# Performance work log

Measured on AMD Instinct MI355X. Metric: run time of the kernel, lower is better.

Reference implementation:

```python
import jax, jax.numpy as jnp
import numpy as np

D_MODEL = 1024
HEADS = 16
D_K = D_MODEL // HEADS  # 64
LN_EPS = 1e-5


def setup_inputs() -> dict:
    key = jax.random.key(0)
    ks = jax.random.split(key, 9)
    B, S = 4, 2048
    x = jax.random.normal(ks[0], (B, S, D_MODEL), dtype=jnp.float32)
    s = 1.0 / np.sqrt(D_K)
    # Per-head linear weights, stacked over heads: [H, d_in, d_out]
    Wq = jax.random.uniform(ks[1], (HEADS, D_K, D_K), jnp.float32, -s, s)
    Wk = jax.random.uniform(ks[2], (HEADS, D_K, D_K), jnp.float32, -s, s)
    Wv = jax.random.uniform(ks[3], (HEADS, D_K, D_K), jnp.float32, -s, s)
    bq = jax.random.uniform(ks[4], (HEADS, D_K), jnp.float32, -s, s)
    bk = jax.random.uniform(ks[5], (HEADS, D_K), jnp.float32, -s, s)
    bv = jax.random.uniform(ks[6], (HEADS, D_K), jnp.float32, -s, s)
    gamma = jnp.ones((D_MODEL,), jnp.float32)
    beta = jnp.zeros((D_MODEL,), jnp.float32)
    return {"x": x, "Wq": Wq, "Wk": Wk, "Wv": Wv,
            "bq": bq, "bk": bk, "bv": bv, "gamma": gamma, "beta": beta}


def reference(x, Wq, Wk, Wv, bq, bk, bv, gamma, beta):
    B, S, D = x.shape
    scale = jnp.sqrt(jnp.asarray(D_K, x.dtype))
    # chunk(x, heads, -1) == reshape to [B,S,H,d_k]
    xh = x.reshape(B, S, HEADS, D_K)
    # Batched per-head linears (replaces the Python loop over heads)
    Q = jnp.einsum('bshd,hde->bshe', xh, Wq) + bq  # [B,S,H,d_k]
    K = jnp.einsum('bshd,hde->bshe', xh, Wk) + bk
    V = jnp.einsum('bshd,hde->bshe', xh, Wv) + bv
    scores = jnp.einsum('bshd,bthd->bhst', Q, K) / scale  # [B,H,S,S]
    A = jax.nn.softmax(scores, axis=-1)
    out = jnp.einsum('bhst,bthd->bshd', A, V).reshape(B, S, D)
    # dropout is identity in eval mode; residual + LayerNorm
    y = out + x
    mu = jnp.mean(y, axis=-1, keepdims=True)
    var = jnp.mean((y - mu) ** 2, axis=-1, keepdims=True)
    return (y - mu) * jax.lax.rsqrt(var + LN_EPS) * gamma + beta
```

## Files before the change

### kernel.cpp

```cpp
#include <hip/hip_runtime.h>
#include <math.h>

typedef __bf16 bf16_t;
typedef __bf16 bf16x8 __attribute__((ext_vector_type(8)));
typedef __bf16 bf16x4 __attribute__((ext_vector_type(4)));
typedef short short4v __attribute__((ext_vector_type(4)));
typedef float f32x4 __attribute__((ext_vector_type(4)));

#define LOG2E 1.4426950408889634f

#if __has_builtin(__builtin_amdgcn_exp2f)
#define FAST_EXP2(x) __builtin_amdgcn_exp2f(x)
#else
#define FAST_EXP2(x) exp2f(x)
#endif

#define GLOBAL_AS __attribute__((address_space(1)))
#define LDS_AS    __attribute__((address_space(3)))

__device__ __forceinline__ void async_ld16(const void* g, void* l) {
    __builtin_amdgcn_global_load_lds((const GLOBAL_AS void*)g,
                                     (LDS_AS void*)l, 16, 0, 0);
}

constexpr int BATCH = 4;
constexpr int SEQ = 2048;
constexpr int NHEADS = 16;
constexpr int DK = 64;
constexpr int DMODEL = 1024;
constexpr int NTOK = BATCH * SEQ;

constexpr size_t WT_OFF   = 0;
constexpr size_t BIAS_OFF = WT_OFF + (size_t)3*16*64*64*2;
constexpr size_t Q_OFF    = BIAS_OFF + (size_t)3*16*64*4;
constexpr size_t QSZ      = (size_t)BATCH*NHEADS*SEQ*DK*2;
constexpr size_t K_OFF    = Q_OFF + QSZ;
constexpr size_t VT_OFF   = K_OFF + QSZ;
constexpr size_t O_OFF    = VT_OFF + QSZ;

__global__ __launch_bounds__(256) void prep_kernel(
    const float* __restrict__ Wq, const float* __restrict__ Wk,
    const float* __restrict__ Wv, const float* __restrict__ bq,
    const float* __restrict__ bk, const float* __restrict__ bv,
    bf16_t* __restrict__ Wt, float* __restrict__ bias)
{
    const float QS = 0.125f * LOG2E;
    int i = blockIdx.x * 256 + threadIdx.x;
    if (i < 3*16*64*64) {
        int d = i & 63, e = (i >> 6) & 63, h = (i >> 12) & 15, p = i >> 16;
        const float* W = (p == 0) ? Wq : (p == 1) ? Wk : Wv;
        float v = W[(h*64 + d)*64 + e] * ((p == 0) ? QS : 1.0f);
        Wt[i] = (bf16_t)v;
    }
    if (i < 3*16*64) {
        int e = i & 63, h = (i >> 6) & 15, p = i >> 10;
        const float* bb = (p == 0) ? bq : (p == 1) ? bk : bv;
        bias[i] = bb[h*64 + e] * ((p == 0) ? QS : 1.0f);
    }
}

__global__ __launch_bounds__(256) void qkv_kernel(
    const float* __restrict__ x, const bf16_t* __restrict__ Wt,
    const float* __restrict__ bias,
    bf16_t* __restrict__ Q, bf16_t* __restrict__ Kg, bf16_t* __restrict__ Vt)
{
    constexpr int QSTR = 72;
    __shared__ bf16_t Slds[4][16 * QSTR];
    const int tid = threadIdx.x;
    const int w = tid >> 6, lane = tid & 63;
    const int ln = lane & 15, quad = lane >> 4;
    const int gw = blockIdx.x * 4 + w;
    const int h = gw & 15, tt = gw >> 4;
    const int t0 = tt * 16;
    const int b = t0 >> 11;
    const int s0 = t0 & 2047;
    const int bh = b * 16 + h;

    bf16x8 afrag[2];
#pragma unroll
    for (int kc = 0; kc < 2; kc++) {
        const float* xp = &x[(size_t)(t0 + ln)*DMODEL + h*DK + kc*32 + quad*8];
        float4 u0 = *(const float4*)xp;
        float4 u1 = *(const float4*)(xp + 4);
        bf16x8 a;
        a[0]=(bf16_t)u0.x; a[1]=(bf16_t)u0.y; a[2]=(bf16_t)u0.z; a[3]=(bf16_t)u0.w;
        a[4]=(bf16_t)u1.x; a[5]=(bf16_t)u1.y; a[6]=(bf16_t)u1.z; a[7]=(bf16_t)u1.w;
        afrag[kc] = a;
    }

#pragma unroll
    for (int p = 0; p < 3; p++) {
#pragma unroll
        for (int nt = 0; nt < 4; nt++) {
            const bf16_t* wp = &Wt[((size_t)((p*16 + h)*64) + nt*16 + ln)*64 + quad*8];
            bf16x8 b0 = *(const bf16x8*)wp;
            bf16x8 b1 = *(const bf16x8*)(wp + 32);
            f32x4 acc = {0.f, 0.f, 0.f, 0.f};
            acc = __builtin_amdgcn_mfma_f32_16x16x32_bf16(afrag[0], b0, acc, 0, 0, 0);
            acc = __builtin_amdgcn_mfma_f32_16x16x32_bf16(afrag[1], b1, acc, 0, 0, 0);
            float bv = bias[(p*16 + h)*64 + nt*16 + ln];
#pragma unroll
            for (int r = 0; r < 4; r++)
                Slds[w][(quad*4 + r)*QSTR + nt*16 + ln] = (bf16_t)(acc[r] + bv);
        }
        if (p < 2) {
            bf16_t* dst = (p == 0) ? Q : Kg;
            const int row = lane >> 2, c = (lane & 3) * 16;
            bf16_t* dp = &dst[((size_t)bh*SEQ + s0 + row)*DK + c];
            *(uint4*)dp       = *(const uint4*)&Slds[w][row*QSTR + c];
            *(uint4*)(dp + 8) = *(const uint4*)&Slds[w][row*QSTR + c + 8];
        } else {
            unsigned int packed[8];
#pragma unroll
            for (int i = 0; i < 8; i++) {
                unsigned short lo = __builtin_bit_cast(unsigned short, Slds[w][(2*i  )*QSTR + lane]);
                unsigned short hi = __builtin_bit_cast(unsigned short, Slds[w][(2*i+1)*QSTR + lane]);
                packed[i] = (unsigned)lo | ((unsigned)hi << 16);
            }
            bf16_t* vp = &Vt[((size_t)bh*DK + lane)*SEQ + s0];
            uint4 v0; v0.x = packed[0]; v0.y = packed[1]; v0.z = packed[2]; v0.w = packed[3];
            uint4 v1; v1.x = packed[4]; v1.y = packed[5]; v1.z = packed[6]; v1.w = packed[7];
            *(uint4*)(vp)     = v0;
            *(uint4*)(vp + 8) = v1;
        }
    }
}

__global__ __launch_bounds__(256, 4) void flash_kernel(
    const bf16_t* __restrict__ Q, const bf16_t* __restrict__ Kg,
    const bf16_t* __restrict__ Vt, bf16_t* __restrict__ O)
{
    __shared__ union {
        struct { bf16_t K[2][64*64]; bf16_t V[2][64*64]; } kv;
        bf16_t O[4][32 * 72];
    } sh;

    const int tid = threadIdx.x;
    const int w = tid >> 6, lane = tid & 63;
    const int ln = lane & 15, quad = lane >> 4;
    const int bid = blockIdx.x;
    const int xcd = bid & 7;
    const int j   = bid >> 3;
    const int bh  = xcd * 8 + (j & 7);
    const int qt  = j >> 3;
    const int q0 = qt * 128 + w * 32;

    const bf16_t* kbase = &Kg[(size_t)bh * SEQ * DK];
    const bf16_t* vbase = &Vt[(size_t)bh * DK * SEQ];

    const int lrow = lane >> 3;
    const int swz  = ((lane & 7) ^ lrow) * 8;

    auto stage = [&](int ci, int buf) {
#pragma unroll
        for (int jj = 0; jj < 2; jj++) {
            const int r = w*16 + jj*8 + lrow;
            async_ld16(&kbase[(size_t)(ci*64 + r)*DK + swz],
                       &sh.kv.K[buf][(w*16 + jj*8)*64]);
            async_ld16(&vbase[(size_t)r*SEQ + ci*64 + swz],
                       &sh.kv.V[buf][(w*16 + jj*8)*64]);
        }
    };

    bf16x8 qfrag[2][2];
#pragma unroll
    for (int st = 0; st < 2; st++)
#pragma unroll
        for (int kc = 0; kc < 2; kc++)
            qfrag[st][kc] = *(const bf16x8*)
                &Q[((size_t)bh*SEQ + q0 + st*16 + ln)*DK + kc*32 + quad*8];

    f32x4 o[2][4];
#pragma unroll
    for (int st = 0; st < 2; st++)
#pragma unroll
        for (int dt = 0; dt < 4; dt++)
            o[st][dt] = (f32x4){0.f, 0.f, 0.f, 0.f};
    float l_[2] = {0.f, 0.f};

    const int s7  = ln & 7;
    const int kc0 = (quad ^ s7) * 8;
    const int vq  = quad >> 1;
    const int vo  = (quad & 1) * 4;

    constexpr int NC = SEQ / 64;
    stage(0, 0);

#pragma unroll 2
    for (int ci = 0; ci < NC; ci++) {
        asm volatile("s_waitcnt vmcnt(0)" ::: "memory");
        __syncthreads();
        if (ci + 1 < NC) stage(ci + 1, (ci + 1) & 1);

        const bf16_t* Kb = sh.kv.K[ci & 1];
        const bf16_t* Vb = sh.kv.V[ci & 1];

        f32x4 sfrag[2][4];
#pragma unroll
        for (int kt = 0; kt < 4; kt++) {
            const int kr = (kt*16 + ln) * 64;
            bf16x8 ka0 = *(const bf16x8*)&Kb[kr + kc0];
            bf16x8 ka1 = *(const bf16x8*)&Kb[kr + (kc0 ^ 32)];
#pragma unroll
            for (int st = 0; st < 2; st++) {
                f32x4 acc = {0.f, 0.f, 0.f, 0.f};
                acc = __builtin_amdgcn_mfma_f32_16x16x32_bf16(ka0, qfrag[st][0], acc, 0, 0, 0);
                acc = __builtin_amdgcn_mfma_f32_16x16x32_bf16(ka1, qfrag[st][1], acc, 0, 0, 0);
                sfrag[st][kt] = acc;
            }
        }

        bf16x8 pfrag[2][2];
#pragma unroll
        for (int st = 0; st < 2; st++) {
            float sum = 0.f;
            unsigned pk[8];
#pragma unroll
            for (int kt = 0; kt < 4; kt++) {
                float e0 = FAST_EXP2(sfrag[st][kt][0]);
                float e1 = FAST_EXP2(sfrag[st][kt][1]);
                float e2 = FAST_EXP2(sfrag[st][kt][2]);
                float e3 = FAST_EXP2(sfrag[st][kt][3]);
                sum += (e0 + e1) + (e2 + e3);
                unsigned u0 = __builtin_bit_cast(unsigned, e0);
                unsigned u1 = __builtin_bit_cast(unsigned, e1);
                unsigned u2 = __builtin_bit_cast(unsigned, e2);
                unsigned u3 = __builtin_bit_cast(unsigned, e3);
                pk[2*kt]     = __builtin_amdgcn_perm(u1, u0, 0x07060302);
                pk[2*kt + 1] = __builtin_amdgcn_perm(u3, u2, 0x07060302);
            }
            l_[st] += sum;
            uint4 lo; lo.x = pk[0]; lo.y = pk[1]; lo.z = pk[2]; lo.w = pk[3];
            uint4 hi; hi.x = pk[4]; hi.y = pk[5]; hi.z = pk[6]; hi.w = pk[7];
            pfrag[st][0] = __builtin_bit_cast(bf16x8, lo);
            pfrag[st][1] = __builtin_bit_cast(bf16x8, hi);
        }

#pragma unroll
        for (int kt2 = 0; kt2 < 2; kt2++) {
#pragma unroll
            for (int dt = 0; dt < 4; dt++) {
                const int vr = (dt*16 + ln) * 64;
                uint2 va0 = *(const uint2*)
                    &Vb[vr + (((kt2*4 + vq) ^ s7) * 8) + vo];
                uint2 va1 = *(const uint2*)
                    &Vb[vr + (((kt2*4 + 2 + vq) ^ s7) * 8) + vo];
                uint4 vv; vv.x = va0.x; vv.y = va0.y; vv.z = va1.x; vv.w = va1.y;
                bf16x8 va = __builtin_bit_cast(bf16x8, vv);
                o[0][dt] = __builtin_amdgcn_mfma_f32_16x16x32_bf16(
                    va, pfrag[0][kt2], o[0][dt], 0, 0, 0);
                o[1][dt] = __builtin_amdgcn_mfma_f32_16x16x32_bf16(
                    va, pfrag[1][kt2], o[1][dt], 0, 0, 0);
            }
        }
    }

    __syncthreads();
#pragma unroll
    for (int st = 0; st < 2; st++) {
        float l = l_[st];
        l += __shfl_xor(l, 16);
        l += __shfl_xor(l, 32);
        float rl = 1.0f / l;
#pragma unroll
        for (int dt = 0; dt < 4; dt++)
#pragma unroll
            for (int r = 0; r < 4; r++)
                sh.O[w][(st*16 + ln)*72 + dt*16 + quad*4 + r] =
                    (bf16_t)(o[st][dt][r] * rl);
    }
    const int token = lane >> 1, half = lane & 1;
    const int b = bh >> 4, h = bh & 15;
    const size_t s = (size_t)q0 + token;
    bf16_t* op = &O[(((size_t)b*SEQ + s)*NHEADS + h)*DK + half*32];
#pragma unroll
    for (int k2 = 0; k2 < 4; k2++)
        *(uint4*)(op + k2*8) = *(const uint4*)&sh.O[w][token*72 + half*32 + k2*8];
}

__global__ __launch_bounds__(256) void ln_kernel(
    const bf16_t* __restrict__ O, const float* __restrict__ x,
    const float* __restrict__ gamma, const float* __restrict__ beta,
    float* __restrict__ out)
{
    const int tid = threadIdx.x;
    const int w = tid >> 6, lane = tid & 63;
    const size_t t = (size_t)blockIdx.x * 4 + w;
    const int d0 = lane * 16;
    const bf16_t* op = &O[t*DMODEL + d0];
    const float* xp = &x[t*DMODEL + d0];

    bf16x8 oa = *(const bf16x8*)op;
    bf16x8 ob = *(const bf16x8*)(op + 8);
    float xs[16];
    ((float4*)xs)[0] = *(const float4*)(xp);
    ((float4*)xs)[1] = *(const float4*)(xp + 4);
    ((float4*)xs)[2] = *(const float4*)(xp + 8);
    ((float4*)xs)[3] = *(const float4*)(xp + 12);

    float yv[16];
    float sum = 0.f, sq = 0.f;
#pragma unroll
    for (int j = 0; j < 16; j++) {
        float ov = (j < 8) ? (float)oa[j] : (float)ob[j - 8];
        yv[j] = ov + xs[j];
        sum += yv[j];
        sq += yv[j] * yv[j];
    }
#pragma unroll
    for (int off = 1; off < 64; off <<= 1) {
        sum += __shfl_xor(sum, off);
        sq  += __shfl_xor(sq, off);
    }
    float mean = sum * (1.0f / DMODEL);
    float var = sq * (1.0f / DMODEL) - mean * mean;
    float rstd = rsqrtf(var + 1e-5f);

    float gs[16], bs[16];
    ((float4*)gs)[0] = *(const float4*)&gamma[d0];
    ((float4*)gs)[1] = *(const float4*)&gamma[d0 + 4];
    ((float4*)gs)[2] = *(const float4*)&gamma[d0 + 8];
    ((float4*)gs)[3] = *(const float4*)&gamma[d0 + 12];
    ((float4*)bs)[0] = *(const float4*)&beta[d0];
    ((float4*)bs)[1] = *(const float4*)&beta[d0 + 4];
    ((float4*)bs)[2] = *(const float4*)&beta[d0 + 8];
    ((float4*)bs)[3] = *(const float4*)&beta[d0 + 12];

    float res[16];
#pragma unroll
    for (int j = 0; j < 16; j++)
        res[j] = (yv[j] - mean) * rstd * gs[j] + bs[j];
    float* outp = &out[t*DMODEL + d0];
    *(float4*)(outp)      = *(float4*)&res[0];
    *(float4*)(outp + 4)  = *(float4*)&res[4];
    *(float4*)(outp + 8)  = *(float4*)&res[8];
    *(float4*)(outp + 12) = *(float4*)&res[12];
}

extern "C" void kernel_launch(void* const* d_in, const int* in_sizes, int n_in,
                              void* d_out, int out_size, void* d_ws, size_t ws_size,
                              hipStream_t stream) {
    const float* x     = (const float*)d_in[0];
    const float* Wq    = (const float*)d_in[1];
    const float* Wk    = (const float*)d_in[2];
    const float* Wv    = (const float*)d_in[3];
    const float* bq    = (const float*)d_in[4];
    const float* bk    = (const float*)d_in[5];
    const float* bv    = (const float*)d_in[6];
    const float* gamma = (const float*)d_in[7];
    const float* beta  = (const float*)d_in[8];

    char* ws = (char*)d_ws;
    bf16_t* Wt   = (bf16_t*)(ws + WT_OFF);
    float*  bias = (float*)(ws + BIAS_OFF);
    bf16_t* Qb   = (bf16_t*)(ws + Q_OFF);
    bf16_t* Kb   = (bf16_t*)(ws + K_OFF);
    bf16_t* Vtb  = (bf16_t*)(ws + VT_OFF);
    bf16_t* Ob   = (bf16_t*)(ws + O_OFF);

    prep_kernel<<<768, 256, 0, stream>>>(Wq, Wk, Wv, bq, bk, bv, Wt, bias);
    qkv_kernel<<<NTOK*NHEADS/16/4, 256, 0, stream>>>(x, Wt, bias, Qb, Kb, Vtb);
    flash_kernel<<<BATCH*NHEADS*(SEQ/128), 256, 0, stream>>>(Qb, Kb, Vtb, Ob);
    ln_kernel<<<NTOK/4, 256, 0, stream>>>(Ob, x, gamma, beta, (float*)d_out);
}
```

Measured before the change: 221.7 us.

## Software-pipeline QK^T ahead of softmax/PV with triple-buffered V and repacked V layout

Restructures the flash attention main loop so that QK^T for the next key chunk is computed while the softmax and PV for the current chunk proceed. A third V buffer and a two-chunk prefetch distance keep loads ahead of compute, and s_setprio is raised around the PV MFMAs. The V-transpose writer also stores V in an interleaved 32-column layout, so the PV A-fragment becomes one 16-byte LDS read instead of two 8-byte reads. The cost is more LDS and higher register pressure from keeping two score tiles live, which could hurt occupancy under the 256x4 launch bounds.

```diff
diff --git a/kernel.cpp b/kernel.cpp
--- a/kernel.cpp
+++ b/kernel.cpp
@@ -117,11 +117,14 @@
                 unsigned short hi = __builtin_bit_cast(unsigned short, Slds[w][(2*i+1)*QSTR + lane]);
                 packed[i] = (unsigned)lo | ((unsigned)hi << 16);
             }
-            bf16_t* vp = &Vt[((size_t)bh*DK + lane)*SEQ + s0];
-            uint4 v0; v0.x = packed[0]; v0.y = packed[1]; v0.z = packed[2]; v0.w = packed[3];
-            uint4 v1; v1.x = packed[4]; v1.y = packed[5]; v1.z = packed[6]; v1.w = packed[7];
-            *(uint4*)(vp)     = v0;
-            *(uint4*)(vp + 8) = v1;
+            const int base32 = s0 & ~31;
+            const int pr = (s0 >> 4) & 1;
+            unsigned* vp32 = (unsigned*)&Vt[((size_t)bh*DK + lane)*SEQ + base32];
+#pragma unroll
+            for (int i2 = 0; i2 < 4; i2++) {
+                uint2 u; u.x = packed[2*i2]; u.y = packed[2*i2 + 1];
+                *(uint2*)(vp32 + i2*4 + pr*2) = u;
+            }
         }
     }
 }
@@ -131,7 +134,7 @@
     const bf16_t* __restrict__ Vt, bf16_t* __restrict__ O)
 {
     __shared__ union {
-        struct { bf16_t K[2][64*64]; bf16_t V[2][64*64]; } kv;
+        struct { bf16_t K[2][64*64]; bf16_t V[3][64*64]; } kv;
         bf16_t O[4][32 * 72];
     } sh;
 
@@ -151,14 +154,18 @@
     const int lrow = lane >> 3;
     const int swz  = ((lane & 7) ^ lrow) * 8;
 
-    auto stage = [&](int ci, int buf) {
+    auto stageK = [&](int ci, bf16_t* dst) {
 #pragma unroll
         for (int jj = 0; jj < 2; jj++) {
             const int r = w*16 + jj*8 + lrow;
-            async_ld16(&kbase[(size_t)(ci*64 + r)*DK + swz],
-                       &sh.kv.K[buf][(w*16 + jj*8)*64]);
-            async_ld16(&vbase[(size_t)r*SEQ + ci*64 + swz],
-                       &sh.kv.V[buf][(w*16 + jj*8)*64]);
+            async_ld16(&kbase[(size_t)(ci*64 + r)*DK + swz], dst + (w*16 + jj*8)*64);
+        }
+    };
+    auto stageV = [&](int ci, bf16_t* dst) {
+#pragma unroll
+        for (int jj = 0; jj < 2; jj++) {
+            const int r = w*16 + jj*8 + lrow;
+            async_ld16(&vbase[(size_t)r*SEQ + ci*64 + swz], dst + (w*16 + jj*8)*64);
         }
     };
 
@@ -180,22 +187,10 @@
 
     const int s7  = ln & 7;
     const int kc0 = (quad ^ s7) * 8;
-    const int vq  = quad >> 1;
-    const int vo  = (quad & 1) * 4;
 
     constexpr int NC = SEQ / 64;
-    stage(0, 0);
-
-#pragma unroll 2
-    for (int ci = 0; ci < NC; ci++) {
-        asm volatile("s_waitcnt vmcnt(0)" ::: "memory");
-        __syncthreads();
-        if (ci + 1 < NC) stage(ci + 1, (ci + 1) & 1);
-
-        const bf16_t* Kb = sh.kv.K[ci & 1];
-        const bf16_t* Vb = sh.kv.V[ci & 1];
-
-        f32x4 sfrag[2][4];
+
+    auto qkt = [&](const bf16_t* Kb, f32x4 (&sf)[2][4]) {
 #pragma unroll
         for (int kt = 0; kt < 4; kt++) {
             const int kr = (kt*16 + ln) * 64;
@@ -206,21 +201,22 @@
                 f32x4 acc = {0.f, 0.f, 0.f, 0.f};
                 acc = __builtin_amdgcn_mfma_f32_16x16x32_bf16(ka0, qfrag[st][0], acc, 0, 0, 0);
                 acc = __builtin_amdgcn_mfma_f32_16x16x32_bf16(ka1, qfrag[st][1], acc, 0, 0, 0);
-                sfrag[st][kt] = acc;
-            }
-        }
-
-        bf16x8 pfrag[2][2];
+                sf[st][kt] = acc;
+            }
+        }
+    };
+
+    auto sm = [&](f32x4 (&sf)[2][4], bf16x8 (&pf)[2][2]) {
 #pragma unroll
         for (int st = 0; st < 2; st++) {
             float sum = 0.f;
             unsigned pk[8];
 #pragma unroll
             for (int kt = 0; kt < 4; kt++) {
-                float e0 = FAST_EXP2(sfrag[st][kt][0]);
-                float e1 = FAST_EXP2(sfrag[st][kt][1]);
-                float e2 = FAST_EXP2(sfrag[st][kt][2]);
-                float e3 = FAST_EXP2(sfrag[st][kt][3]);
+                float e0 = FAST_EXP2(sf[st][kt][0]);
+                float e1 = FAST_EXP2(sf[st][kt][1]);
+                float e2 = FAST_EXP2(sf[st][kt][2]);
+                float e3 = FAST_EXP2(sf[st][kt][3]);
                 sum += (e0 + e1) + (e2 + e3);
                 unsigned u0 = __builtin_bit_cast(unsigned, e0);
                 unsigned u1 = __builtin_bit_cast(unsigned, e1);
@@ -232,26 +228,62 @@
             l_[st] += sum;
             uint4 lo; lo.x = pk[0]; lo.y = pk[1]; lo.z = pk[2]; lo.w = pk[3];
             uint4 hi; hi.x = pk[4]; hi.y = pk[5]; hi.z = pk[6]; hi.w = pk[7];
-            pfrag[st][0] = __builtin_bit_cast(bf16x8, lo);
-            pfrag[st][1] = __builtin_bit_cast(bf16x8, hi);
-        }
-
+            pf[st][0] = __builtin_bit_cast(bf16x8, lo);
+            pf[st][1] = __builtin_bit_cast(bf16x8, hi);
+        }
+    };
+
+    auto pv = [&](const bf16_t* Vb, bf16x8 (&pf)[2][2]) {
 #pragma unroll
         for (int kt2 = 0; kt2 < 2; kt2++) {
 #pragma unroll
             for (int dt = 0; dt < 4; dt++) {
                 const int vr = (dt*16 + ln) * 64;
-                uint2 va0 = *(const uint2*)
-                    &Vb[vr + (((kt2*4 + vq) ^ s7) * 8) + vo];
-                uint2 va1 = *(const uint2*)
-                    &Vb[vr + (((kt2*4 + 2 + vq) ^ s7) * 8) + vo];
-                uint4 vv; vv.x = va0.x; vv.y = va0.y; vv.z = va1.x; vv.w = va1.y;
-                bf16x8 va = __builtin_bit_cast(bf16x8, vv);
+                bf16x8 va = *(const bf16x8*)&Vb[vr + (((kt2*4 + quad) ^ s7) * 8)];
                 o[0][dt] = __builtin_amdgcn_mfma_f32_16x16x32_bf16(
-                    va, pfrag[0][kt2], o[0][dt], 0, 0, 0);
+                    va, pf[0][kt2], o[0][dt], 0, 0, 0);
                 o[1][dt] = __builtin_amdgcn_mfma_f32_16x16x32_bf16(
-                    va, pfrag[1][kt2], o[1][dt], 0, 0, 0);
-            }
+                    va, pf[1][kt2], o[1][dt], 0, 0, 0);
+            }
+        }
+    };
+
+    stageK(0, sh.kv.K[0]); stageV(0, sh.kv.V[0]);
+    stageK(1, sh.kv.K[1]); stageV(1, sh.kv.V[1]);
+    __syncthreads();
+
+    f32x4 sA[2][4], sB[2][4];
+    qkt(sh.kv.K[0], sA);
+
+    bf16_t* vcur = sh.kv.V[0];
+    bf16_t* vnxt = sh.kv.V[1];
+    bf16_t* vfar = sh.kv.V[2];
+
+    for (int cc = 0; cc < NC; cc += 2) {
+        {
+            asm volatile("s_waitcnt vmcnt(0)" ::: "memory");
+            __syncthreads();
+            if (cc + 2 < NC) { stageK(cc + 2, sh.kv.K[0]); stageV(cc + 2, vfar); }
+            bf16x8 pf[2][2];
+            sm(sA, pf);
+            qkt(sh.kv.K[1], sB);
+            __builtin_amdgcn_s_setprio(1);
+            pv(vcur, pf);
+            __builtin_amdgcn_s_setprio(0);
+            bf16_t* t = vcur; vcur = vnxt; vnxt = vfar; vfar = t;
+        }
+        {
+            const int c = cc + 1;
+            asm volatile("s_waitcnt vmcnt(0)" ::: "memory");
+            __syncthreads();
+            if (c + 2 < NC) { stageK(c + 2, sh.kv.K[1]); stageV(c + 2, vfar); }
+            bf16x8 pf[2][2];
+            sm(sB, pf);
+            if (c + 1 < NC) qkt(sh.kv.K[0], sA);
+            __builtin_amdgcn_s_setprio(1);
+            pv(vcur, pf);
+            __builtin_amdgcn_s_setprio(0);
+            bf16_t* t = vcur; vcur = vnxt; vnxt = vfar; vfar = t;
         }
     }
 
```

New measurement: 625.7 us. +182.2%, slower.

## Permute V layout to match MFMA fragments, stage x tile in LDS, raise MFMA priority

Applied to the files above, without the earlier changes.

The QKV kernel now has each block cover four heads of a 16-token tile. It loads the x tile cooperatively into LDS as bf16, so global reads are coalesced and contiguous. V^T is written in an interleaved per-32-token layout so the flash kernel can load each V fragment as one 16-byte LDS read instead of two 8-byte reads. The PV MFMA loop is wrapped in s_setprio to favour matrix issue. This adds a block barrier and a second LDS buffer in the QKV kernel, and it relies on the producer and consumer agreeing on the permuted V layout.

```diff
diff --git a/kernel.cpp b/kernel.cpp
--- a/kernel.cpp
+++ b/kernel.cpp
@@ -65,28 +65,37 @@
     bf16_t* __restrict__ Q, bf16_t* __restrict__ Kg, bf16_t* __restrict__ Vt)
 {
     constexpr int QSTR = 72;
+    constexpr int XSTR = 264;
+    __shared__ bf16_t Xlds[16 * XSTR];
     __shared__ bf16_t Slds[4][16 * QSTR];
     const int tid = threadIdx.x;
     const int w = tid >> 6, lane = tid & 63;
     const int ln = lane & 15, quad = lane >> 4;
-    const int gw = blockIdx.x * 4 + w;
-    const int h = gw & 15, tt = gw >> 4;
-    const int t0 = tt * 16;
+    const int bid = blockIdx.x;
+    const int t0 = (bid >> 2) * 16;
+    const int h0 = (bid & 3) * 4;
+    const int h  = h0 + w;
     const int b = t0 >> 11;
     const int s0 = t0 & 2047;
     const int bh = b * 16 + h;
 
+#pragma unroll
+    for (int i = 0; i < 4; i++) {
+        const int idx = i * 256 + tid;
+        const int row = idx >> 6;
+        const int c4  = idx & 63;
+        float4 u = *(const float4*)&x[(size_t)(t0 + row)*DMODEL + h0*64 + c4*4];
+        bf16x4 v4;
+        v4[0] = (bf16_t)u.x; v4[1] = (bf16_t)u.y;
+        v4[2] = (bf16_t)u.z; v4[3] = (bf16_t)u.w;
+        *(bf16x4*)&Xlds[row*XSTR + c4*4] = v4;
+    }
+    __syncthreads();
+
     bf16x8 afrag[2];
 #pragma unroll
-    for (int kc = 0; kc < 2; kc++) {
-        const float* xp = &x[(size_t)(t0 + ln)*DMODEL + h*DK + kc*32 + quad*8];
-        float4 u0 = *(const float4*)xp;
-        float4 u1 = *(const float4*)(xp + 4);
-        bf16x8 a;
-        a[0]=(bf16_t)u0.x; a[1]=(bf16_t)u0.y; a[2]=(bf16_t)u0.z; a[3]=(bf16_t)u0.w;
-        a[4]=(bf16_t)u1.x; a[5]=(bf16_t)u1.y; a[6]=(bf16_t)u1.z; a[7]=(bf16_t)u1.w;
-        afrag[kc] = a;
-    }
+    for (int kc = 0; kc < 2; kc++)
+        afrag[kc] = *(const bf16x8*)&Xlds[ln*XSTR + w*64 + kc*32 + quad*8];
 
 #pragma unroll
     for (int p = 0; p < 3; p++) {
@@ -117,11 +126,14 @@
                 unsigned short hi = __builtin_bit_cast(unsigned short, Slds[w][(2*i+1)*QSTR + lane]);
                 packed[i] = (unsigned)lo | ((unsigned)hi << 16);
             }
-            bf16_t* vp = &Vt[((size_t)bh*DK + lane)*SEQ + s0];
-            uint4 v0; v0.x = packed[0]; v0.y = packed[1]; v0.z = packed[2]; v0.w = packed[3];
-            uint4 v1; v1.x = packed[4]; v1.y = packed[5]; v1.z = packed[6]; v1.w = packed[7];
-            *(uint4*)(vp)     = v0;
-            *(uint4*)(vp + 8) = v1;
+            const int base32 = s0 & ~31;
+            const int pr = (s0 >> 4) & 1;
+            unsigned* vp32 = (unsigned*)&Vt[((size_t)bh*DK + lane)*SEQ + base32];
+#pragma unroll
+            for (int i2 = 0; i2 < 4; i2++) {
+                uint2 u; u.x = packed[2*i2]; u.y = packed[2*i2 + 1];
+                *(uint2*)(vp32 + i2*4 + pr*2) = u;
+            }
         }
     }
 }
@@ -180,8 +192,6 @@
 
     const int s7  = ln & 7;
     const int kc0 = (quad ^ s7) * 8;
-    const int vq  = quad >> 1;
-    const int vo  = (quad & 1) * 4;
 
     constexpr int NC = SEQ / 64;
     stage(0, 0);
@@ -236,23 +246,20 @@
             pfrag[st][1] = __builtin_bit_cast(bf16x8, hi);
         }
 
+        __builtin_amdgcn_s_setprio(1);
 #pragma unroll
         for (int kt2 = 0; kt2 < 2; kt2++) {
 #pragma unroll
             for (int dt = 0; dt < 4; dt++) {
                 const int vr = (dt*16 + ln) * 64;
-                uint2 va0 = *(const uint2*)
-                    &Vb[vr + (((kt2*4 + vq) ^ s7) * 8) + vo];
-                uint2 va1 = *(const uint2*)
-                    &Vb[vr + (((kt2*4 + 2 + vq) ^ s7) * 8) + vo];
-                uint4 vv; vv.x = va0.x; vv.y = va0.y; vv.z = va1.x; vv.w = va1.y;
-                bf16x8 va = __builtin_bit_cast(bf16x8, vv);
+                bf16x8 va = *(const bf16x8*)&Vb[vr + (((kt2*4 + quad) ^ s7) * 8)];
                 o[0][dt] = __builtin_amdgcn_mfma_f32_16x16x32_bf16(
                     va, pfrag[0][kt2], o[0][dt], 0, 0, 0);
                 o[1][dt] = __builtin_amdgcn_mfma_f32_16x16x32_bf16(
                     va, pfrag[1][kt2], o[1][dt], 0, 0, 0);
             }
         }
+        __builtin_amdgcn_s_setprio(0);
     }
 
     __syncthreads();
```

Result: no change. 219.3 us (-1.1%).
